# Optimization experiments

Measured on AMD Instinct MI355X. Metric: run time of the kernel, lower is better.

The kernel has to match this reference:

```python
import jax, jax.numpy as jnp
import numpy as np

N_NODES = 100000
N_EDGES = 1600000
IN_DIM, HID_DIM, OUT_DIM = 128, 256, 64


def setup_inputs() -> dict:
    key = jax.random.key(0)
    ks = jax.random.split(key, 8)
    h = jax.random.normal(ks[0], (N_NODES, IN_DIM), dtype=jnp.float32)
    W1 = jax.random.normal(ks[1], (IN_DIM, HID_DIM), dtype=jnp.float32) * (1.0 / np.sqrt(IN_DIM))
    b1 = jnp.zeros((HID_DIM,), dtype=jnp.float32)
    W2 = jax.random.normal(ks[2], (HID_DIM, OUT_DIM), dtype=jnp.float32) * (1.0 / np.sqrt(HID_DIM))
    b2 = jnp.zeros((OUT_DIM,), dtype=jnp.float32)
    p = jax.random.uniform(ks[3], (HID_DIM,), dtype=jnp.float32)  # variational dropout retain probs
    src = jax.random.randint(ks[4], (N_EDGES,), 0, N_NODES, dtype=jnp.int32)
    dst = jax.random.randint(ks[5], (N_EDGES,), 0, N_NODES, dtype=jnp.int32)
    return {"h": h, "W1": W1, "b1": b1, "W2": W2, "b2": b2, "p": p,
            "src": src, "dst": dst, "n_nodes": N_NODES}


def _gcn_norms(src, dst, n_nodes, dtype):
    # DGL GraphConv norm='both': D_out^{-1/2} on source side, D_in^{-1/2} on dest side,
    # degrees clamped to min 1.
    ones = jnp.ones(src.shape, dtype=dtype)
    deg_out = jnp.clip(jax.ops.segment_sum(ones, src, num_segments=n_nodes), 1.0, None)
    deg_in = jnp.clip(jax.ops.segment_sum(ones, dst, num_segments=n_nodes), 1.0, None)
    return deg_out ** -0.5, deg_in ** -0.5


def _spmm(x, src, dst, n_nodes):
    # sum-aggregate src features into dst nodes (copy_u + sum)
    return jax.ops.segment_sum(x[src], dst, num_segments=n_nodes)


def reference(h, W1, b1, W2, b2, p, src, dst, n_nodes):
    norm_src, norm_dst = _gcn_norms(src, dst, n_nodes, h.dtype)

    # --- GraphConv 1 (in 128 <= out 256: aggregate first, then weight) ---
    x = h * norm_src[:, None]
    x = _spmm(x, src, dst, n_nodes)              # [N, IN_DIM]
    x = x * norm_dst[:, None]
    x = x @ W1 + b1                               # [N, HID_DIM]
    x = jax.nn.relu(x)

    # --- deterministic variational dropout: scale by clamp(p, 0, 1) ---
    x = x * jnp.clip(p, 0.0, 1.0)[None, :]

    # --- GraphConv 2 (in 256 > out 64: weight first, then aggregate) ---
    y = x @ W2                                    # [N, OUT_DIM]
    y = y * norm_src[:, None]
    y = _spmm(y, src, dst, n_nodes)
    y = y * norm_dst[:, None] + b2
    return y
```

## Files before the change

kernel.cpp:

```cpp
#include <hip/hip_runtime.h>

#define IN_DIM 128
#define HID 256
#define OUTD 64
#define NB 256

typedef __attribute__((ext_vector_type(8))) short bf16x8;
typedef __attribute__((ext_vector_type(4))) float f32x4;
typedef __attribute__((ext_vector_type(8))) unsigned short ushort8v;

__device__ __forceinline__ unsigned short f2bf(float x) {
    unsigned int u = __float_as_uint(x);
    unsigned int r = (u + 0x7fffu + ((u >> 16) & 1u)) >> 16;
    return (unsigned short)r;
}
__device__ __forceinline__ float bf2f(unsigned short b) {
    return __uint_as_float(((unsigned int)b) << 16);
}


__global__ __launch_bounds__(256) void k_bucketA(const int* __restrict__ src,
                                                 const int* __restrict__ dst,
                                                 int* __restrict__ partS, int* __restrict__ partD,
                                                 int E, int NBK) {
    __shared__ int hS[512], hD[512];
    int b = blockIdx.x, t = threadIdx.x;
    for (int j = t; j < 512; j += 256) { hS[j] = 0; hD[j] = 0; }
    __syncthreads();
    int chunk = (E + NB - 1) / NB;
    int e0 = b * chunk, e1 = min(E, e0 + chunk);
    for (int e = e0 + t; e < e1; e += 256) {
        atomicAdd(&hS[src[e] >> 8], 1);
        atomicAdd(&hD[dst[e] >> 8], 1);
    }
    __syncthreads();
    for (int j = t; j < NBK; j += 256) {
        partS[j * NB + b] = hS[j];
        partD[j * NB + b] = hD[j];
    }
}

__global__ __launch_bounds__(512) void k_bscan2(int* __restrict__ partS, int* __restrict__ partD,
                                                int* __restrict__ sOff, int* __restrict__ dOff,
                                                int* __restrict__ eoff,
                                                int N, int E, int NBK) {
    __shared__ int sS[512], sD[512];
    int t = threadIdx.x;
    int totS = 0, totD = 0;
    if (t < NBK) {
        for (int b = 0; b < NB; ++b) { totS += partS[t * NB + b]; totD += partD[t * NB + b]; }
    }
    sS[t] = totS; sD[t] = totD;
    __syncthreads();
    for (int o = 1; o < 512; o <<= 1) {
        int xS = (t >= o) ? sS[t - o] : 0;
        int xD = (t >= o) ? sD[t - o] : 0;
        __syncthreads();
        sS[t] += xS; sD[t] += xD;
        __syncthreads();
    }
    if (t < NBK) {
        int runS = sS[t] - totS, runD = sD[t] - totD;
        sOff[t] = runS; dOff[t] = runD;
        for (int b = 0; b < NB; ++b) {
            int vS = partS[t * NB + b]; partS[t * NB + b] = runS; runS += vS;
            int vD = partD[t * NB + b]; partD[t * NB + b] = runD; runD += vD;
        }
    }
    if (t == 0) { sOff[NBK] = E; dOff[NBK] = E; eoff[N] = E; }
}

__global__ __launch_bounds__(256) void k_bucketB2(const int* __restrict__ src,
                                                  const int* __restrict__ dst,
                                                  const int* __restrict__ partS,
                                                  const int* __restrict__ partD,
                                                  unsigned int* __restrict__ dpairs,
                                                  unsigned char* __restrict__ sloc,
                                                  int E, int NBK) {
    __shared__ int cS[512], cD[512];
    int b = blockIdx.x, t = threadIdx.x;
    for (int j = t; j < NBK; j += 256) {
        cS[j] = partS[j * NB + b];
        cD[j] = partD[j * NB + b];
    }
    __syncthreads();
    int chunk = (E + NB - 1) / NB;
    int e0 = b * chunk, e1 = min(E, e0 + chunk);
    for (int e = e0 + t; e < e1; e += 256) {
        int s = src[e], d = dst[e];
        int pD = atomicAdd(&cD[d >> 8], 1);
        dpairs[pD] = ((unsigned int)(d & 255) << 17) | (unsigned int)s;
        int pS = atomicAdd(&cS[s >> 8], 1);
        sloc[pS] = (unsigned char)(s & 255);
    }
}

__global__ __launch_bounds__(256) void k_bucketC(const unsigned int* __restrict__ dpairs,
                                                 const int* __restrict__ dOff,
                                                 int* __restrict__ eoff,
                                                 int* __restrict__ esrc,
                                                 float* __restrict__ nd,
                                                 int N) {
    __shared__ int hist[256], sc[256], cur[256];
    int b = blockIdx.x, t = threadIdx.x;
    int base = dOff[b], end = dOff[b + 1];
    hist[t] = 0;
    __syncthreads();
    for (int i = base + t; i < end; i += 256)
        atomicAdd(&hist[dpairs[i] >> 17], 1);
    __syncthreads();
    int cnt = hist[t];
    int v = b * 256 + t;
    if (v < N) nd[v] = rsqrtf((float)max(cnt, 1));
    sc[t] = cnt;
    __syncthreads();
    for (int o = 1; o < 256; o <<= 1) {
        int x = (t >= o) ? sc[t - o] : 0;
        __syncthreads();
        sc[t] += x;
        __syncthreads();
    }
    int excl = sc[t] - cnt;
    if (v < N) eoff[v] = base + excl;
    cur[t] = excl;
    __syncthreads();
    for (int i = base + t; i < end; i += 256) {
        unsigned int pk = dpairs[i];
        int pos = atomicAdd(&cur[pk >> 17], 1);
        esrc[base + pos] = (int)(pk & 0x1FFFFu);
    }
}

__global__ __launch_bounds__(256) void k_bucketCs(const unsigned char* __restrict__ sloc,
                                                  const int* __restrict__ sOff,
                                                  float* __restrict__ ns,
                                                  int N) {
    __shared__ int hist[256];
    int b = blockIdx.x, t = threadIdx.x;
    int base = sOff[b], end = sOff[b + 1];
    hist[t] = 0;
    __syncthreads();
    for (int i = base + t; i < end; i += 256)
        atomicAdd(&hist[sloc[i]], 1);
    __syncthreads();
    int v = b * 256 + t;
    if (v < N) ns[v] = rsqrtf((float)max(hist[t], 1));
}

__global__ void k_hconv(const float* __restrict__ h, const float* __restrict__ ns,
                        unsigned short* __restrict__ hb, int total4) {
    int i = blockIdx.x * 256 + threadIdx.x;
    if (i >= total4) return;
    int node = i >> 5;
    float nsv = ns[node];
    float4 v = ((const float4*)h)[i];
    ushort4 o;
    o.x = f2bf(v.x * nsv);
    o.y = f2bf(v.y * nsv);
    o.z = f2bf(v.z * nsv);
    o.w = f2bf(v.w * nsv);
    ((ushort4*)hb)[i] = o;
}

__global__ void k_wprep(const float* __restrict__ W1, const float* __restrict__ W2,
                        unsigned short* __restrict__ Wt1, unsigned short* __restrict__ Wt2) {
    int t = blockIdx.x * 256 + threadIdx.x;
    if (t < IN_DIM * HID) {
        int k = t & (IN_DIM - 1), n = t >> 7;
        Wt1[(size_t)n * IN_DIM + k] = f2bf(W1[(size_t)k * HID + n]);
    }
    if (t < HID * OUTD) {
        int k = t & (HID - 1), n = t >> 8;
        Wt2[(size_t)n * HID + k] = f2bf(W2[(size_t)k * OUTD + n]);
    }
}

__global__ __launch_bounds__(256) void k_spmm1(const unsigned short* __restrict__ hb,
                                               const int* __restrict__ eoff,
                                               const int* __restrict__ esrc,
                                               const float* __restrict__ nd,
                                               unsigned short* __restrict__ xb, int N) {
    int wid = threadIdx.x >> 6;
    int v = blockIdx.x * 4 + wid;
    if (v >= N) return;
    int l = threadIdx.x & 63;
    int c = l & 15, el = l >> 4;
    int s0 = eoff[v], s1 = eoff[v + 1];

    float a0[8] = {0.f, 0.f, 0.f, 0.f, 0.f, 0.f, 0.f, 0.f};
    float a1[8] = {0.f, 0.f, 0.f, 0.f, 0.f, 0.f, 0.f, 0.f};
    int i = s0 + el;
    for (; i + 4 < s1; i += 8) {
        int sA = esrc[i], sB = esrc[i + 4];
        ushort8v uA = *(const ushort8v*)(hb + (size_t)sA * IN_DIM + c * 8);
        ushort8v uB = *(const ushort8v*)(hb + (size_t)sB * IN_DIM + c * 8);
#pragma unroll
        for (int k = 0; k < 8; ++k) {
            a0[k] += bf2f((unsigned short)uA[k]);
            a1[k] += bf2f((unsigned short)uB[k]);
        }
    }
    for (; i < s1; i += 4) {
        int sA = esrc[i];
        ushort8v uA = *(const ushort8v*)(hb + (size_t)sA * IN_DIM + c * 8);
#pragma unroll
        for (int k = 0; k < 8; ++k) a0[k] += bf2f((unsigned short)uA[k]);
    }
    float s[8];
#pragma unroll
    for (int k = 0; k < 8; ++k) {
        float x = a0[k] + a1[k];
        x += __shfl_xor(x, 16);
        x += __shfl_xor(x, 32);
        s[k] = x;
    }
    if (el == 0) {
        float ndv = nd[v];
        uint4 o;
        unsigned int* op = (unsigned int*)&o;
#pragma unroll
        for (int k = 0; k < 4; ++k) {
            unsigned int lo = f2bf(s[2 * k] * ndv);
            unsigned int hi = f2bf(s[2 * k + 1] * ndv);
            op[k] = lo | (hi << 16);
        }
        *(uint4*)(xb + (size_t)v * IN_DIM + c * 8) = o;
    }
}

template <int EPI>
__global__ __launch_bounds__(256) void k_mgemm(const unsigned short* __restrict__ A,
                                               const unsigned short* __restrict__ Bt,
                                               const float* __restrict__ b1,
                                               const float* __restrict__ p,
                                               const float* __restrict__ ns,
                                               unsigned short* __restrict__ outp,
                                               int M) {
    constexpr int BM = (EPI == 1) ? 64 : 256;
    constexpr int BN = (EPI == 1) ? 256 : 64;
    constexpr int K = (EPI == 1) ? 128 : 256;
    constexpr int OUT_LD = (EPI == 1) ? 256 : 64;
    __shared__ unsigned short As[BM * 64];
    __shared__ unsigned short Bs[BN * 64];
    const int t = threadIdx.x, w = t >> 6, l = t & 63;
    const int row0 = blockIdx.x * BM;
    const int wm0 = (EPI == 1) ? 0 : w * 64;
    const int wn0 = (EPI == 1) ? w * 64 : 0;
    const int lr = l & 15, lk = (l >> 4) * 8, lg = l >> 4;

    f32x4 acc[4][4] = {};

    for (int k0 = 0; k0 < K; k0 += 64) {
#pragma unroll
        for (int q = 0; q < BM / 32; ++q) {
            int chunk = w * (BM / 32) + q;
            int gr = row0 + chunk * 8 + (l >> 3);
            if (gr > M - 1) gr = M - 1;
            const unsigned short* gp = A + (size_t)gr * K + k0 + (l & 7) * 8;
            __builtin_amdgcn_global_load_lds((const __attribute__((address_space(1))) void*)gp,
                                             (__attribute__((address_space(3))) void*)&As[chunk * 512], 16, 0, 0);
        }
#pragma unroll
        for (int q = 0; q < BN / 32; ++q) {
            int chunk = w * (BN / 32) + q;
            int r = chunk * 8 + (l >> 3);
            const unsigned short* gp = Bt + (size_t)r * K + k0 + (l & 7) * 8;
            __builtin_amdgcn_global_load_lds((const __attribute__((address_space(1))) void*)gp,
                                             (__attribute__((address_space(3))) void*)&Bs[chunk * 512], 16, 0, 0);
        }
        __syncthreads();

#pragma unroll
        for (int kk = 0; kk < 2; ++kk) {
            bf16x8 a[4], b[4];
#pragma unroll
            for (int m = 0; m < 4; ++m)
                a[m] = *(const bf16x8*)&As[(wm0 + m * 16 + lr) * 64 + kk * 32 + lk];
#pragma unroll
            for (int n = 0; n < 4; ++n)
                b[n] = *(const bf16x8*)&Bs[(wn0 + n * 16 + lr) * 64 + kk * 32 + lk];
#pragma unroll
            for (int m = 0; m < 4; ++m)
#pragma unroll
                for (int n = 0; n < 4; ++n)
                    acc[m][n] = __builtin_amdgcn_mfma_f32_16x16x32_bf16(a[m], b[n], acc[m][n], 0, 0, 0);
        }
        __syncthreads();
    }

#pragma unroll
    for (int n = 0; n < 4; ++n) {
        int col = wn0 + n * 16 + lr;
        float bb = 0.f, pp = 1.f;
        if (EPI == 1) {
            bb = b1[col];
            pp = fminf(fmaxf(p[col], 0.f), 1.f);
        }
#pragma unroll
        for (int m = 0; m < 4; ++m) {
#pragma unroll
            for (int j = 0; j < 4; ++j) {
                int row = row0 + wm0 + m * 16 + lg * 4 + j;
                if (row < M) {
                    float v = acc[m][n][j];
                    if (EPI == 1) {
                        v = fmaxf(v + bb, 0.f) * pp;
                    } else {
                        v *= ns[row];
                    }
                    outp[(size_t)row * OUT_LD + col] = f2bf(v);
                }
            }
        }
    }
}

__global__ __launch_bounds__(256) void k_spmm2(const unsigned short* __restrict__ ybf,
                                               const int* __restrict__ eoff,
                                               const int* __restrict__ esrc,
                                               const float* __restrict__ nd,
                                               const float* __restrict__ b2,
                                               float* __restrict__ out, int N) {
    int wid = threadIdx.x >> 6;
    int v = blockIdx.x * 4 + wid;
    if (v >= N) return;
    int l = threadIdx.x & 63;
    int c = l & 15, el = l >> 4;
    int s0 = eoff[v], s1 = eoff[v + 1];

    float ax0 = 0.f, ay0 = 0.f, az0 = 0.f, aw0 = 0.f;
    float ax1 = 0.f, ay1 = 0.f, az1 = 0.f, aw1 = 0.f;
    int i = s0 + el;
    for (; i + 4 < s1; i += 8) {
        int sA = esrc[i], sB = esrc[i + 4];
        ushort4 uA = *(const ushort4*)(ybf + (size_t)sA * OUTD + c * 4);
        ushort4 uB = *(const ushort4*)(ybf + (size_t)sB * OUTD + c * 4);
        ax0 += bf2f(uA.x); ay0 += bf2f(uA.y); az0 += bf2f(uA.z); aw0 += bf2f(uA.w);
        ax1 += bf2f(uB.x); ay1 += bf2f(uB.y); az1 += bf2f(uB.z); aw1 += bf2f(uB.w);
    }
    for (; i < s1; i += 4) {
        ushort4 u = *(const ushort4*)(ybf + (size_t)esrc[i] * OUTD + c * 4);
        ax0 += bf2f(u.x); ay0 += bf2f(u.y); az0 += bf2f(u.z); aw0 += bf2f(u.w);
    }
    float ax = ax0 + ax1, ay = ay0 + ay1, az = az0 + az1, aw = aw0 + aw1;
    ax += __shfl_xor(ax, 16); ax += __shfl_xor(ax, 32);
    ay += __shfl_xor(ay, 16); ay += __shfl_xor(ay, 32);
    az += __shfl_xor(az, 16); az += __shfl_xor(az, 32);
    aw += __shfl_xor(aw, 16); aw += __shfl_xor(aw, 32);
    if (l < 16) {
        float ndv = nd[v];
        float4 bb = *(const float4*)(b2 + c * 4);
        float4 o;
        o.x = ax * ndv + bb.x;
        o.y = ay * ndv + bb.y;
        o.z = az * ndv + bb.z;
        o.w = aw * ndv + bb.w;
        *(float4*)(out + (size_t)v * OUTD + c * 4) = o;
    }
}

extern "C" void kernel_launch(void* const* d_in, const int* in_sizes, int n_in,
                              void* d_out, int out_size, void* d_ws, size_t ws_size,
                              hipStream_t stream) {
    const float* h  = (const float*)d_in[0];
    const float* W1 = (const float*)d_in[1];
    const float* b1 = (const float*)d_in[2];
    const float* W2 = (const float*)d_in[3];
    const float* b2 = (const float*)d_in[4];
    const float* p  = (const float*)d_in[5];
    const int* src  = (const int*)d_in[6];
    const int* dst  = (const int*)d_in[7];

    const int N = in_sizes[0] / IN_DIM;
    const int E = in_sizes[6];
    const int NBK = (N + 255) >> 8;
    float* out = (float*)d_out;

    char* ws = (char*)d_ws;
    size_t off = 0;
    auto alloc = [&](size_t bytes) -> void* {
        void* ptr = ws + off;
        off = (off + bytes + 255) & ~(size_t)255;
        return ptr;
    };
    int* sOff = (int*)alloc(513 * 4);
    int* dOff = (int*)alloc(513 * 4);
    int* eoff = (int*)alloc((size_t)(N + 1) * 4);
    int* esrc = (int*)alloc((size_t)E * 4);
    float* ns = (float*)alloc((size_t)N * 4);
    float* nd = (float*)alloc((size_t)N * 4);
    unsigned short* hb  = (unsigned short*)alloc((size_t)N * IN_DIM * 2);
    unsigned short* xb  = (unsigned short*)alloc((size_t)N * IN_DIM * 2);
    unsigned short* hid = (unsigned short*)alloc((size_t)N * HID * 2);
    unsigned short* Wt1 = (unsigned short*)alloc((size_t)HID * IN_DIM * 2);
    unsigned short* Wt2 = (unsigned short*)alloc((size_t)OUTD * HID * 2);
    unsigned short* ybf = xb;
    unsigned int* dpairs = (unsigned int*)hid;
    unsigned char* sloc  = (unsigned char*)hid + (size_t)E * 4;
    int* partS = (int*)((char*)hid + ((size_t)E * 5 + 255 & ~(size_t)255));
    int* partD = partS + 512 * NB;

    int tpb = 256;
    k_bucketA<<<NB, 256, 0, stream>>>(src, dst, partS, partD, E, NBK);
    k_bscan2<<<1, 512, 0, stream>>>(partS, partD, sOff, dOff, eoff, N, E, NBK);
    k_bucketB2<<<NB, 256, 0, stream>>>(src, dst, partS, partD, dpairs, sloc, E, NBK);
    k_bucketC<<<NBK, 256, 0, stream>>>(dpairs, dOff, eoff, esrc, nd, N);
    k_bucketCs<<<NBK, 256, 0, stream>>>(sloc, sOff, ns, N);

    int total4 = N * (IN_DIM / 4);
    k_hconv<<<(total4 + tpb - 1) / tpb, tpb, 0, stream>>>(h, ns, hb, total4);

    k_wprep<<<(IN_DIM * HID + 255) / 256, 256, 0, stream>>>(W1, W2, Wt1, Wt2);

    k_spmm1<<<(N + 3) / 4, 256, 0, stream>>>(hb, eoff, esrc, nd, xb, N);

    k_mgemm<1><<<(N + 63) / 64, 256, 0, stream>>>(xb, Wt1, b1, p, nullptr, hid, N);

    k_mgemm<2><<<(N + 255) / 256, 256, 0, stream>>>(hid, Wt2, nullptr, nullptr, ns, ybf, N);

    k_spmm2<<<(N + 3) / 4, 256, 0, stream>>>(ybf, eoff, esrc, nd, b2, out, N);
}
```

Baseline: 426.5 us.

## Parallelize bucket offset scan across blocks instead of single-block serial loops

Replaces the single-block scan, which had each of up to 512 threads serially walk 256 partition counts twice, with a two-level scan. One block per bucket scans its 256 per-block counts in parallel, then a single block scans the bucket totals. The global bucket base is added when bucketB2 loads its counters. This removes a serial, strided, single-CU bottleneck at the cost of one extra kernel launch.

```diff
diff --git a/kernel.cpp b/kernel.cpp
--- a/kernel.cpp
+++ b/kernel.cpp
@@ -40,17 +40,35 @@
     }
 }
 
-__global__ __launch_bounds__(512) void k_bscan2(int* __restrict__ partS, int* __restrict__ partD,
+__global__ __launch_bounds__(256) void k_bscanP(int* __restrict__ partS, int* __restrict__ partD,
+                                                int* __restrict__ totS, int* __restrict__ totD) {
+    __shared__ int sS[256], sD[256];
+    int j = blockIdx.x, t = threadIdx.x;
+    int vS = partS[j * NB + t], vD = partD[j * NB + t];
+    sS[t] = vS; sD[t] = vD;
+    __syncthreads();
+    for (int o = 1; o < 256; o <<= 1) {
+        int xS = (t >= o) ? sS[t - o] : 0;
+        int xD = (t >= o) ? sD[t - o] : 0;
+        __syncthreads();
+        sS[t] += xS; sD[t] += xD;
+        __syncthreads();
+    }
+    partS[j * NB + t] = sS[t] - vS;
+    partD[j * NB + t] = sD[t] - vD;
+    if (t == 255) { totS[j] = sS[255]; totD[j] = sD[255]; }
+}
+
+__global__ __launch_bounds__(512) void k_bscanT(const int* __restrict__ totS,
+                                                const int* __restrict__ totD,
                                                 int* __restrict__ sOff, int* __restrict__ dOff,
                                                 int* __restrict__ eoff,
                                                 int N, int E, int NBK) {
     __shared__ int sS[512], sD[512];
     int t = threadIdx.x;
-    int totS = 0, totD = 0;
-    if (t < NBK) {
-        for (int b = 0; b < NB; ++b) { totS += partS[t * NB + b]; totD += partD[t * NB + b]; }
-    }
-    sS[t] = totS; sD[t] = totD;
+    int vS = (t < NBK) ? totS[t] : 0;
+    int vD = (t < NBK) ? totD[t] : 0;
+    sS[t] = vS; sD[t] = vD;
     __syncthreads();
     for (int o = 1; o < 512; o <<= 1) {
         int xS = (t >= o) ? sS[t - o] : 0;
@@ -59,14 +77,7 @@
         sS[t] += xS; sD[t] += xD;
         __syncthreads();
     }
-    if (t < NBK) {
-        int runS = sS[t] - totS, runD = sD[t] - totD;
-        sOff[t] = runS; dOff[t] = runD;
-        for (int b = 0; b < NB; ++b) {
-            int vS = partS[t * NB + b]; partS[t * NB + b] = runS; runS += vS;
-            int vD = partD[t * NB + b]; partD[t * NB + b] = runD; runD += vD;
-        }
-    }
+    if (t < NBK) { sOff[t] = sS[t] - vS; dOff[t] = sD[t] - vD; }
     if (t == 0) { sOff[NBK] = E; dOff[NBK] = E; eoff[N] = E; }
 }
 
@@ -74,14 +85,16 @@
                                                   const int* __restrict__ dst,
                                                   const int* __restrict__ partS,
                                                   const int* __restrict__ partD,
+                                                  const int* __restrict__ sOff,
+                                                  const int* __restrict__ dOff,
                                                   unsigned int* __restrict__ dpairs,
                                                   unsigned char* __restrict__ sloc,
                                                   int E, int NBK) {
     __shared__ int cS[512], cD[512];
     int b = blockIdx.x, t = threadIdx.x;
     for (int j = t; j < NBK; j += 256) {
-        cS[j] = partS[j * NB + b];
-        cD[j] = partD[j * NB + b];
+        cS[j] = partS[j * NB + b] + sOff[j];
+        cD[j] = partD[j * NB + b] + dOff[j];
     }
     __syncthreads();
     int chunk = (E + NB - 1) / NB;
@@ -385,6 +398,8 @@
     };
     int* sOff = (int*)alloc(513 * 4);
     int* dOff = (int*)alloc(513 * 4);
+    int* totS = (int*)alloc(512 * 4);
+    int* totD = (int*)alloc(512 * 4);
     int* eoff = (int*)alloc((size_t)(N + 1) * 4);
     int* esrc = (int*)alloc((size_t)E * 4);
     float* ns = (float*)alloc((size_t)N * 4);
@@ -402,8 +417,9 @@
 
     int tpb = 256;
     k_bucketA<<<NB, 256, 0, stream>>>(src, dst, partS, partD, E, NBK);
-    k_bscan2<<<1, 512, 0, stream>>>(partS, partD, sOff, dOff, eoff, N, E, NBK);
-    k_bucketB2<<<NB, 256, 0, stream>>>(src, dst, partS, partD, dpairs, sloc, E, NBK);
+    k_bscanP<<<NBK, 256, 0, stream>>>(partS, partD, totS, totD);
+    k_bscanT<<<1, 512, 0, stream>>>(totS, totD, sOff, dOff, eoff, N, E, NBK);
+    k_bucketB2<<<NB, 256, 0, stream>>>(src, dst, partS, partD, sOff, dOff, dpairs, sloc, E, NBK);
     k_bucketC<<<NBK, 256, 0, stream>>>(dpairs, dOff, eoff, esrc, nd, N);
     k_bucketCs<<<NBK, 256, 0, stream>>>(sloc, sOff, ns, N);
 
```

New measurement: 348.9 us. -18.2%, faster.
